# Kernel tuning notes

Measured on AMD Instinct MI355X. Metric: run time of the kernel, lower is better.

Reference implementation:

```python
import jax, jax.numpy as jnp
import numpy as np

N = 100000      # nodes
E = 3200000     # directed edges
IN = 512
H = 32          # hidden width fixed by the module
OUT = 64
EPS = 1e-5      # BatchNorm1d default eps


def setup_inputs() -> dict:
    key = jax.random.key(0)
    ks = jax.random.split(key, 10)
    x = jax.random.normal(ks[0], (N, IN), dtype=jnp.float32)
    edge_index = jax.random.randint(ks[1], (2, E), 0, N, dtype=jnp.int32)
    # GCNConv params (Linear weight + bias)
    W1 = jax.random.normal(ks[2], (IN, H), dtype=jnp.float32) / np.sqrt(IN)
    b1 = jnp.zeros((H,), dtype=jnp.float32)
    W2 = jax.random.normal(ks[3], (H, OUT), dtype=jnp.float32) / np.sqrt(H)
    b2 = jnp.zeros((OUT,), dtype=jnp.float32)
    # BatchNorm1d(32) params + running stats (eval mode)
    gamma = jax.random.normal(ks[4], (H,), dtype=jnp.float32) * 0.1 + 1.0
    beta = jax.random.normal(ks[5], (H,), dtype=jnp.float32) * 0.1
    running_mean = jax.random.normal(ks[6], (H,), dtype=jnp.float32) * 0.1
    running_var = jax.random.uniform(ks[7], (H,), dtype=jnp.float32, minval=0.5, maxval=1.5)
    return {"x": x, "edge_index": edge_index, "W1": W1, "b1": b1,
            "W2": W2, "b2": b2, "gamma": gamma, "beta": beta,
            "running_mean": running_mean, "running_var": running_var}


def _gcn_norm(edge_index):
    # PyG GCNConv default: add self-loops, symmetric normalization.
    src0, dst0 = edge_index[0], edge_index[1]
    loops = jnp.arange(N, dtype=edge_index.dtype)
    src = jnp.concatenate([src0, loops])
    dst = jnp.concatenate([dst0, loops])
    deg = jax.ops.segment_sum(jnp.ones_like(dst, dtype=jnp.float32), dst, num_segments=N)
    dinv = jnp.where(deg > 0, jax.lax.rsqrt(deg), 0.0)
    norm = dinv[src] * dinv[dst]  # [E+N]
    return src, dst, norm


def _gcn_conv(h, src, dst, norm, b):
    # gather -> scale -> scatter-add, then bias
    msg = h[src] * norm[:, None]
    agg = jax.ops.segment_sum(msg, dst, num_segments=N)
    return agg + b


def reference(x, edge_index, W1, b1, W2, b2, gamma, beta, running_mean, running_var):
    src, dst, norm = _gcn_norm(edge_index)
    h = _gcn_conv(x @ W1, src, dst, norm, b1)              # [N, 32]
    h = (h - running_mean) * jax.lax.rsqrt(running_var + EPS) * gamma + beta
    h = jax.nn.relu(h)
    # dropout is identity in eval mode
    out = _gcn_conv(h @ W2, src, dst, norm, b2)            # [N, 64]
    return out
```

## Files before the change

### kernel.cpp

```cpp
#include <hip/hip_runtime.h>
#include <hip/hip_fp16.h>

#define N_NODES 100000
#define E_EDGES 3200000
#define IN_F 512
#define H_F 32
#define OUT_F 64
#define BN_EPS 1e-5f
#define NBINS 1563
#define CHUNK 16384

struct H8 { __half2 h[4]; };
struct H4 { __half2 a, b; };

__global__ __launch_bounds__(256) void k_prep(const float* __restrict__ gamma,
                                              const float* __restrict__ beta,
                                              const float* __restrict__ rm,
                                              const float* __restrict__ rv,
                                              const float* __restrict__ b1,
                                              float* __restrict__ scale,
                                              float* __restrict__ shift,
                                              unsigned* __restrict__ binCnt,
                                              unsigned* __restrict__ binPos) {
    int t = blockIdx.x * 256 + threadIdx.x;
    if (t < NBINS) { binCnt[t] = 0u; binPos[t] = 0u; }
    if (blockIdx.x == 0 && threadIdx.x < H_F) {
        int k = threadIdx.x;
        float s = gamma[k] * rsqrtf(rv[k] + BN_EPS);
        scale[k] = s;
        shift[k] = (b1[k] - rm[k]) * s + beta[k];
    }
}

__global__ __launch_bounds__(256) void k_hist(const int* __restrict__ dst,
                                              unsigned* __restrict__ binCnt) {
    __shared__ unsigned h[NBINS];
    for (int i = threadIdx.x; i < NBINS; i += 256) h[i] = 0;
    __syncthreads();
    for (int e = blockIdx.x * 256 + threadIdx.x; e < E_EDGES; e += 256 * 512)
        atomicAdd(&h[((unsigned)dst[e]) >> 6], 1u);
    __syncthreads();
    for (int i = threadIdx.x; i < NBINS; i += 256) {
        unsigned v = h[i];
        if (v) atomicAdd(&binCnt[i], v);
    }
}

__global__ __launch_bounds__(256) void k_scanbins(const unsigned* __restrict__ binCnt,
                                                  unsigned* __restrict__ binOff) {
    __shared__ unsigned carry;
    __shared__ unsigned wtot[4];
    if (threadIdx.x == 0) carry = 0;
    __syncthreads();
    int lane = threadIdx.x & 63, wid = threadIdx.x >> 6;
    for (int base = 0; base < NBINS; base += 256) {
        int i = base + (int)threadIdx.x;
        unsigned v = (i < NBINS) ? binCnt[i] : 0u;
        unsigned xs = v;
#pragma unroll
        for (int s = 1; s < 64; s <<= 1) {
            unsigned t = __shfl_up(xs, s, 64);
            if (lane >= s) xs += t;
        }
        if (lane == 63) wtot[wid] = xs;
        __syncthreads();
        unsigned wbase = 0, tot = 0;
#pragma unroll
        for (int w = 0; w < 4; ++w) { if (w < wid) wbase += wtot[w]; tot += wtot[w]; }
        if (i < NBINS) binOff[i] = carry + wbase + xs - v;
        __syncthreads();
        if (threadIdx.x == 0) carry += tot;
        __syncthreads();
    }
}

__global__ __launch_bounds__(256) void k_binfill(const int* __restrict__ src,
                                                 const int* __restrict__ dst,
                                                 const unsigned* __restrict__ binOff,
                                                 unsigned* __restrict__ binPos,
                                                 unsigned* __restrict__ packed) {
    __shared__ unsigned h[NBINS];
    for (int i = threadIdx.x; i < NBINS; i += 256) h[i] = 0;
    __syncthreads();
    int e0 = blockIdx.x * CHUNK;
    int e1 = min(e0 + CHUNK, E_EDGES);
    for (int e = e0 + threadIdx.x; e < e1; e += 256)
        atomicAdd(&h[((unsigned)dst[e]) >> 6], 1u);
    __syncthreads();
    for (int i = threadIdx.x; i < NBINS; i += 256) {
        unsigned c = h[i];
        h[i] = c ? atomicAdd(&binPos[i], c) : 0u;
    }
    __syncthreads();
    for (int e = e0 + threadIdx.x; e < e1; e += 256) {
        unsigned s = (unsigned)src[e];
        unsigned d = (unsigned)dst[e];
        unsigned bin = d >> 6;
        unsigned pos = atomicAdd(&h[bin], 1u);
        packed[binOff[bin] + pos] = ((d & 63u) << 17) | s;
    }
}

__global__ __launch_bounds__(256) void k_sortbin(const unsigned* __restrict__ binOff,
                                                 const unsigned* __restrict__ binCnt,
                                                 const unsigned* __restrict__ packed,
                                                 unsigned* __restrict__ off,
                                                 unsigned* __restrict__ deg,
                                                 float* __restrict__ dinv,
                                                 unsigned* __restrict__ csr) {
    __shared__ unsigned cnt[64];
    __shared__ unsigned cur[64];
    int bin = blockIdx.x;
    if (threadIdx.x < 64) cnt[threadIdx.x] = 0;
    __syncthreads();
    unsigned base = binOff[bin], len = binCnt[bin];
    for (unsigned j = threadIdx.x; j < len; j += 256)
        atomicAdd(&cnt[packed[base + j] >> 17], 1u);
    __syncthreads();
    if (threadIdx.x < 64) {
        unsigned v = cnt[threadIdx.x];
        unsigned xs = v;
#pragma unroll
        for (int s = 1; s < 64; s <<= 1) {
            unsigned t = __shfl_up(xs, s, 64);
            if ((int)threadIdx.x >= s) xs += t;
        }
        unsigned loc = xs - v;
        cur[threadIdx.x] = loc;
        int node = bin * 64 + (int)threadIdx.x;
        if (node < N_NODES) {
            off[node]  = base + loc;
            deg[node]  = v;
            dinv[node] = rsqrtf((float)v + 1.0f);
        }
    }
    __syncthreads();
    for (unsigned j = threadIdx.x; j < len; j += 256) {
        unsigned p = packed[base + j];
        unsigned pos = atomicAdd(&cur[p >> 17], 1u);
        csr[base + pos] = p & 0x1FFFFu;
    }
}

#define TM 128
#define TK 32
__global__ __launch_bounds__(256) void k_gemm1(const float* __restrict__ x,
                                               const float* __restrict__ W1,
                                               const float* __restrict__ dinv,
                                               __half* __restrict__ xw16) {
    __shared__ float xs[TM * TK];
    __shared__ float ws[TK * H_F];
    const int t   = threadIdx.x;
    const int tr  = t >> 3;
    const int tq  = t & 7;
    const int c0  = tq * 4;
    const int swz = tr & 7;
    const int row0 = blockIdx.x * TM;
    float acc[4][4] = {};
    for (int k0 = 0; k0 < IN_F; k0 += TK) {
#pragma unroll
        for (int p = 0; p < 4; ++p) {
            int r = p * 32 + tr;
            int gr = row0 + r;
            if (gr >= N_NODES) gr = N_NODES - 1;
            float4 v = *(const float4*)(x + (size_t)gr * IN_F + k0 + tq * 4);
            *(float4*)&xs[r * TK + ((tq ^ (r & 7)) << 2)] = v;
        }
        {
            float4 v = *(const float4*)(W1 + (size_t)(k0 + tr) * H_F + tq * 4);
            *(float4*)&ws[tr * H_F + tq * 4] = v;
        }
        __syncthreads();
#pragma unroll
        for (int kk = 0; kk < TK; kk += 4) {
            float xr[4][4], wr[4][4];
            const int q = ((kk >> 2) ^ swz) << 2;
#pragma unroll
            for (int i = 0; i < 4; ++i) {
                float4 v = *(const float4*)&xs[(tr + 32 * i) * TK + q];
                xr[i][0] = v.x; xr[i][1] = v.y; xr[i][2] = v.z; xr[i][3] = v.w;
            }
#pragma unroll
            for (int j = 0; j < 4; ++j) {
                float4 v = *(const float4*)&ws[(kk + j) * H_F + c0];
                wr[j][0] = v.x; wr[j][1] = v.y; wr[j][2] = v.z; wr[j][3] = v.w;
            }
#pragma unroll
            for (int k = 0; k < 4; ++k)
#pragma unroll
                for (int i = 0; i < 4; ++i)
#pragma unroll
                    for (int j = 0; j < 4; ++j)
                        acc[i][j] = fmaf(xr[i][k], wr[k][j], acc[i][j]);
        }
        __syncthreads();
    }
#pragma unroll
    for (int i = 0; i < 4; ++i) {
        int r = row0 + tr + 32 * i;
        if (r < N_NODES) {
            float dv = dinv[r];
            H4 o;
            o.a = __floats2half2_rn(acc[i][0] * dv, acc[i][1] * dv);
            o.b = __floats2half2_rn(acc[i][2] * dv, acc[i][3] * dv);
            *(H4*)(xw16 + (size_t)r * H_F + c0) = o;
        }
    }
}

__device__ inline void acc8(float* acc, float4 raw) {
    const __half2* h = (const __half2*)&raw;
#pragma unroll
    for (int j = 0; j < 4; ++j) {
        float2 f = __half22float2(h[j]);
        acc[2 * j]     += f.x;
        acc[2 * j + 1] += f.y;
    }
}

__global__ __launch_bounds__(256) void k_gather1(const unsigned* __restrict__ off,
                                                 const unsigned* __restrict__ deg,
                                                 const unsigned* __restrict__ csr,
                                                 const __half* __restrict__ xw16,
                                                 const float* __restrict__ dinv,
                                                 const float* __restrict__ scale,
                                                 const float* __restrict__ shift,
                                                 __half* __restrict__ hs16) {
    int lane  = threadIdx.x & 63;
    int ll    = lane & 31;
    int g     = ll >> 2;
    int q     = ll & 3;
    int d = blockIdx.x * 8 + ((threadIdx.x >> 6) << 1) + (lane >> 5);
    const unsigned* cp = csr + off[d];
    unsigned n = deg[d];
    float acc[8] = {};
    unsigned i = g;
    for (; i + 24 < n; i += 32) {
        unsigned s0 = cp[i], s1 = cp[i + 8], s2 = cp[i + 16], s3 = cp[i + 24];
        float4 r0 = *(const float4*)(xw16 + (size_t)s0 * H_F + q * 8);
        float4 r1 = *(const float4*)(xw16 + (size_t)s1 * H_F + q * 8);
        float4 r2 = *(const float4*)(xw16 + (size_t)s2 * H_F + q * 8);
        float4 r3 = *(const float4*)(xw16 + (size_t)s3 * H_F + q * 8);
        acc8(acc, r0); acc8(acc, r1); acc8(acc, r2); acc8(acc, r3);
    }
    for (; i < n; i += 8) {
        float4 r = *(const float4*)(xw16 + (size_t)cp[i] * H_F + q * 8);
        acc8(acc, r);
    }
#pragma unroll
    for (int st = 4; st <= 16; st <<= 1)
#pragma unroll
        for (int j = 0; j < 8; ++j)
            acc[j] += __shfl_xor(acc[j], st, 64);
    if (g == 0) {
        float dv = dinv[d];
        float sf[8];
        {
            float4 raw = *(const float4*)(xw16 + (size_t)d * H_F + q * 8);
            const __half2* h = (const __half2*)&raw;
#pragma unroll
            for (int j = 0; j < 4; ++j) {
                float2 f = __half22float2(h[j]);
                sf[2 * j] = f.x; sf[2 * j + 1] = f.y;
            }
        }
        float scf[8], shf[8];
        *(float4*)scf       = *(const float4*)(scale + q * 8);
        *(float4*)(scf + 4) = *(const float4*)(scale + q * 8 + 4);
        *(float4*)shf       = *(const float4*)(shift + q * 8);
        *(float4*)(shf + 4) = *(const float4*)(shift + q * 8 + 4);
        H8 o;
#pragma unroll
        for (int j = 0; j < 4; ++j) {
            float a0 = (acc[2 * j]     + sf[2 * j])     * dv;
            float a1 = (acc[2 * j + 1] + sf[2 * j + 1]) * dv;
            float h0 = fmaxf(fmaf(a0, scf[2 * j],     shf[2 * j]),     0.f) * dv;
            float h1 = fmaxf(fmaf(a1, scf[2 * j + 1], shf[2 * j + 1]), 0.f) * dv;
            o.h[j] = __floats2half2_rn(h0, h1);
        }
        *(H8*)(hs16 + (size_t)d * H_F + q * 8) = o;
    }
}

__global__ __launch_bounds__(256) void k_gather2(const unsigned* __restrict__ off,
                                                 const unsigned* __restrict__ deg,
                                                 const unsigned* __restrict__ csr,
                                                 const __half* __restrict__ hs16,
                                                 const float* __restrict__ dinv,
                                                 const float* __restrict__ W2,
                                                 const float* __restrict__ b2,
                                                 float* __restrict__ out) {
    __shared__ float ws[H_F * OUT_F];
    __shared__ float bs[OUT_F];
    for (int i = threadIdx.x; i < H_F * OUT_F; i += 256) ws[i] = W2[i];
    if (threadIdx.x < OUT_F) bs[threadIdx.x] = b2[threadIdx.x];
    __syncthreads();
    int lane  = threadIdx.x & 63;
    int ll    = lane & 31;
    int g     = ll >> 2;
    int q     = ll & 3;
    int d = blockIdx.x * 8 + ((threadIdx.x >> 6) << 1) + (lane >> 5);
    const unsigned* cp = csr + off[d];
    unsigned n = deg[d];
    float acc[8] = {};
    unsigned i = g;
    for (; i + 24 < n; i += 32) {
        unsigned s0 = cp[i], s1 = cp[i + 8], s2 = cp[i + 16], s3 = cp[i + 24];
        float4 r0 = *(const float4*)(hs16 + (size_t)s0 * H_F + q * 8);
        float4 r1 = *(const float4*)(hs16 + (size_t)s1 * H_F + q * 8);
        float4 r2 = *(const float4*)(hs16 + (size_t)s2 * H_F + q * 8);
        float4 r3 = *(const float4*)(hs16 + (size_t)s3 * H_F + q * 8);
        acc8(acc, r0); acc8(acc, r1); acc8(acc, r2); acc8(acc, r3);
    }
    for (; i < n; i += 8) {
        float4 r = *(const float4*)(hs16 + (size_t)cp[i] * H_F + q * 8);
        acc8(acc, r);
    }
#pragma unroll
    for (int st = 4; st <= 16; st <<= 1)
#pragma unroll
        for (int j = 0; j < 8; ++j)
            acc[j] += __shfl_xor(acc[j], st, 64);
    float tv[8];
#pragma unroll
    for (int j = 0; j < 8; ++j) tv[j] = 0.f;
    if (g == 0) {
        float dv = dinv[d];
        float4 raw = *(const float4*)(hs16 + (size_t)d * H_F + q * 8);
        const __half2* h = (const __half2*)&raw;
#pragma unroll
        for (int j = 0; j < 4; ++j) {
            float2 f = __half22float2(h[j]);
            tv[2 * j]     = (acc[2 * j]     + f.x) * dv;
            tv[2 * j + 1] = (acc[2 * j + 1] + f.y) * dv;
        }
    }
    float o0 = bs[ll], o1 = bs[ll + 32];
#pragma unroll
    for (int k = 0; k < H_F; ++k) {
        float a = __shfl(tv[k & 7], k >> 3, 32);
        o0 = fmaf(a, ws[k * OUT_F + ll],      o0);
        o1 = fmaf(a, ws[k * OUT_F + ll + 32], o1);
    }
    out[(size_t)d * OUT_F + ll]      = o0;
    out[(size_t)d * OUT_F + ll + 32] = o1;
}

extern "C" void kernel_launch(void* const* d_in, const int* in_sizes, int n_in,
                              void* d_out, int out_size, void* d_ws, size_t ws_size,
                              hipStream_t stream) {
    const float* x     = (const float*)d_in[0];
    const int*   ei    = (const int*)d_in[1];
    const float* W1    = (const float*)d_in[2];
    const float* b1    = (const float*)d_in[3];
    const float* W2    = (const float*)d_in[4];
    const float* b2    = (const float*)d_in[5];
    const float* gamma = (const float*)d_in[6];
    const float* beta  = (const float*)d_in[7];
    const float* rm    = (const float*)d_in[8];
    const float* rv    = (const float*)d_in[9];
    float* out = (float*)d_out;

    const int* src = ei;
    const int* dst = ei + E_EDGES;

    __half*   xw16   = (__half*)d_ws;
    __half*   hs16   = xw16 + (size_t)N_NODES * H_F;
    unsigned* packed = (unsigned*)d_ws;
    unsigned* csr    = (unsigned*)(hs16 + (size_t)N_NODES * H_F);
    float*    dinv   = (float*)(csr + E_EDGES);
    unsigned* off    = (unsigned*)(dinv + N_NODES);
    unsigned* deg    = off + N_NODES;
    float*    scale  = (float*)(deg + N_NODES);
    float*    shift  = scale + H_F;
    unsigned* binCnt = (unsigned*)(shift + H_F);
    unsigned* binPos = binCnt + NBINS;
    unsigned* binOff = binPos + NBINS;

    k_prep<<<(NBINS + 255) / 256, 256, 0, stream>>>(gamma, beta, rm, rv, b1,
                                                    scale, shift, binCnt, binPos);
    k_hist<<<512, 256, 0, stream>>>(dst, binCnt);
    k_scanbins<<<1, 256, 0, stream>>>(binCnt, binOff);
    k_binfill<<<(E_EDGES + CHUNK - 1) / CHUNK, 256, 0, stream>>>(src, dst, binOff, binPos, packed);
    k_sortbin<<<NBINS, 256, 0, stream>>>(binOff, binCnt, packed, off, deg, dinv, csr);

    k_gemm1<<<(N_NODES + TM - 1) / TM, 256, 0, stream>>>(x, W1, dinv, xw16);
    k_gather1<<<N_NODES / 8, 256, 0, stream>>>(off, deg, csr, xw16, dinv, scale, shift, hs16);
    k_gather2<<<N_NODES / 8, 256, 0, stream>>>(off, deg, csr, hs16, dinv, W2, b2, out);
}
```

Before: 322.8 us.

## Register-prefetch next GEMM1 tile and unroll histogram loads by four

The x@W1 GEMM kernel now loads the next K-tile of x and W1 into registers while the current tile is being computed, so global-load latency overlaps with FMA work. The edge histogram loop is unrolled four ways so several dst loads are in flight before the shared-memory atomics. Both changes add register pressure, which could lower occupancy. The GEMM is bandwidth bound on reading 200MB of x, so the gain depends on how much latency the existing occupancy already hid.

```diff
diff --git a/kernel.cpp b/kernel.cpp
--- a/kernel.cpp
+++ b/kernel.cpp
@@ -37,7 +37,19 @@
     __shared__ unsigned h[NBINS];
     for (int i = threadIdx.x; i < NBINS; i += 256) h[i] = 0;
     __syncthreads();
-    for (int e = blockIdx.x * 256 + threadIdx.x; e < E_EDGES; e += 256 * 512)
+    const int stride = 256 * 512;
+    int e = blockIdx.x * 256 + threadIdx.x;
+    for (; e + 3 * stride < E_EDGES; e += 4 * stride) {
+        unsigned d0 = (unsigned)dst[e];
+        unsigned d1 = (unsigned)dst[e + stride];
+        unsigned d2 = (unsigned)dst[e + 2 * stride];
+        unsigned d3 = (unsigned)dst[e + 3 * stride];
+        atomicAdd(&h[d0 >> 6], 1u);
+        atomicAdd(&h[d1 >> 6], 1u);
+        atomicAdd(&h[d2 >> 6], 1u);
+        atomicAdd(&h[d3 >> 6], 1u);
+    }
+    for (; e < E_EDGES; e += stride)
         atomicAdd(&h[((unsigned)dst[e]) >> 6], 1u);
     __syncthreads();
     for (int i = threadIdx.x; i < NBINS; i += 256) {
@@ -156,21 +168,38 @@
     const int c0  = tq * 4;
     const int swz = tr & 7;
     const int row0 = blockIdx.x * TM;
+
+    int grs[4];
+#pragma unroll
+    for (int p = 0; p < 4; ++p) {
+        int gr = row0 + p * 32 + tr;
+        grs[p] = (gr >= N_NODES) ? (N_NODES - 1) : gr;
+    }
+
+    float4 rx[4], rw;
+#pragma unroll
+    for (int p = 0; p < 4; ++p)
+        rx[p] = *(const float4*)(x + (size_t)grs[p] * IN_F + tq * 4);
+    rw = *(const float4*)(W1 + (size_t)tr * H_F + tq * 4);
+
     float acc[4][4] = {};
     for (int k0 = 0; k0 < IN_F; k0 += TK) {
 #pragma unroll
         for (int p = 0; p < 4; ++p) {
             int r = p * 32 + tr;
-            int gr = row0 + r;
-            if (gr >= N_NODES) gr = N_NODES - 1;
-            float4 v = *(const float4*)(x + (size_t)gr * IN_F + k0 + tq * 4);
-            *(float4*)&xs[r * TK + ((tq ^ (r & 7)) << 2)] = v;
-        }
-        {
-            float4 v = *(const float4*)(W1 + (size_t)(k0 + tr) * H_F + tq * 4);
-            *(float4*)&ws[tr * H_F + tq * 4] = v;
-        }
+            *(float4*)&xs[r * TK + ((tq ^ (r & 7)) << 2)] = rx[p];
+        }
+        *(float4*)&ws[tr * H_F + tq * 4] = rw;
         __syncthreads();
+
+        if (k0 + TK < IN_F) {
+            int kn = k0 + TK;
+#pragma unroll
+            for (int p = 0; p < 4; ++p)
+                rx[p] = *(const float4*)(x + (size_t)grs[p] * IN_F + kn + tq * 4);
+            rw = *(const float4*)(W1 + (size_t)(kn + tr) * H_F + tq * 4);
+        }
+
 #pragma unroll
         for (int kk = 0; kk < TK; kk += 4) {
             float xr[4][4], wr[4][4];
```

After: 372.3 us. +15.3%, slower.
